# Performance work log

Hardware: AMD Instinct MI355X
Metric: run time of the kernel (lower is better)

## Reference

```python
import jax, jax.numpy as jnp
import numpy as np

N = 100000
E = 1600000
F_NODE = 32
F_EDGE = 8
H = 64


def _lin_params(key, fan_in, fan_out):
    k1, k2 = jax.random.split(key)
    lim = 1.0 / np.sqrt(fan_in)
    W = jax.random.uniform(k1, (fan_in, fan_out), minval=-lim, maxval=lim, dtype=jnp.float32)
    b = jax.random.uniform(k2, (fan_out,), minval=-lim, maxval=lim, dtype=jnp.float32)
    return W, b


def setup_inputs() -> dict:
    key = jax.random.key(0)
    ks = jax.random.split(key, 8)
    x = jax.random.normal(ks[0], (N, F_NODE), dtype=jnp.float32)
    edge_index = jax.random.randint(ks[1], (2, E), 0, N, dtype=jnp.int64)
    edge_attr = jax.random.normal(ks[2], (E, F_EDGE), dtype=jnp.float32)
    W_embed, b_embed = _lin_params(ks[3], F_NODE, H)
    W_c1, b_c1 = _lin_params(ks[4], H, H)
    W_c2, b_c2 = _lin_params(ks[5], H, H)
    W_p1, b_p1 = _lin_params(ks[6], 2 * H + F_EDGE, H)
    W_p2, b_p2 = _lin_params(ks[7], H, 1)
    return dict(x=x, edge_attr=edge_attr, W_embed=W_embed, b_embed=b_embed,
                W_c1=W_c1, b_c1=b_c1, W_c2=W_c2, b_c2=b_c2,
                W_p1=W_p1, b_p1=b_p1, W_p2=W_p2, b_p2=b_p2,
                edge_index=edge_index)


def gcn_conv(h, W, b, src, dst, n):
    # PyG GCNConv: add self-loops, symmetric normalization, then scatter-sum.
    h = h @ W  # [N, H]
    loops = jnp.arange(n, dtype=src.dtype)
    s = jnp.concatenate([src, loops])
    d = jnp.concatenate([dst, loops])
    deg = jax.ops.segment_sum(jnp.ones_like(d, dtype=h.dtype), d, num_segments=n)
    dinv = jnp.where(deg > 0, jax.lax.rsqrt(deg), 0.0)
    norm = dinv[s] * dinv[d]  # [E+N]
    msg = h[s] * norm[:, None]  # gather source features
    out = jax.ops.segment_sum(msg, d, num_segments=n)  # scatter to targets
    return out + b


def reference(x, edge_attr, W_embed, b_embed, W_c1, b_c1, W_c2, b_c2,
              W_p1, b_p1, W_p2, b_p2, edge_index):
    src, dst = edge_index[0], edge_index[1]
    h = jax.nn.relu(x @ W_embed + b_embed)
    h = jax.nn.relu(gcn_conv(h, W_c1, b_c1, src, dst, N))
    h = jax.nn.relu(gcn_conv(h, W_c2, b_c2, src, dst, N))
    # edge-level gather + concat with edge attrs
    ef = jnp.concatenate([h[src], h[dst], edge_attr], axis=1)  # [E, 2H+Fe]
    z = jax.nn.relu(ef @ W_p1 + b_p1)
    out = (z @ W_p2 + b_p2).squeeze(1)  # [E]
    return out
```

## Files before the change

kernel.cpp:

```cpp
#include <hip/hip_runtime.h>
#include <hip/hip_fp16.h>


typedef __attribute__((ext_vector_type(8))) _Float16 half8;
typedef __attribute__((ext_vector_type(4))) float f32x4;

__device__ __forceinline__ unsigned short f2h(float f) {
    return __half_as_ushort(__float2half(f));
}
__device__ __forceinline__ float h2f(unsigned short u) {
    return __half2float(__ushort_as_half(u));
}

__global__ void detect_idx_k(const unsigned int* __restrict__ ei, int* __restrict__ flag) {
    int nz = 0;
    for (int i = threadIdx.x; i < 2048; i += 64)
        if (ei[2 * i + 1] != 0u) nz = 1;
    unsigned long long m = __ballot(nz);
    if (threadIdx.x == 0) *flag = (m != 0ull) ? 1 : 0;
}

__global__ void cvt_idx_k(const void* __restrict__ ei, const int* __restrict__ flag,
                          int* __restrict__ out, int n) {
    int i = blockIdx.x * 256 + threadIdx.x;
    if (i >= n) return;
    if (*flag) out[i] = ((const int*)ei)[i];
    else       out[i] = (int)((const long long*)ei)[i];
}

__global__ void deg_i_k(const int* __restrict__ dst, int* __restrict__ deg, int E) {
    int i = blockIdx.x * 256 + threadIdx.x;
    if (i < E) atomicAdd(&deg[dst[i]], 1);
}

__global__ void scan_blk_k(const int* __restrict__ deg, int* __restrict__ part,
                           int* __restrict__ bsum, int n1) {
    __shared__ int s[256];
    int t = threadIdx.x;
    int i = blockIdx.x * 256 + t;
    int v = (i < n1) ? deg[i] : 0;
    s[t] = v;
    __syncthreads();
    for (int o = 1; o < 256; o <<= 1) {
        int x = (t >= o) ? s[t - o] : 0;
        __syncthreads();
        s[t] += x;
        __syncthreads();
    }
    if (i < n1) part[i] = s[t] - v;
    if (t == 255) bsum[blockIdx.x] = s[255];
}

__global__ void scan_tot_k(int* __restrict__ bsum, int nb) {
    __shared__ int s[512];
    int t = threadIdx.x;
    int v = (t < nb) ? bsum[t] : 0;
    s[t] = v;
    __syncthreads();
    for (int o = 1; o < 512; o <<= 1) {
        int x = (t >= o) ? s[t - o] : 0;
        __syncthreads();
        s[t] += x;
        __syncthreads();
    }
    if (t < nb) bsum[t] = s[t] - v;
}

__global__ void scan_add_k(const int* __restrict__ part, const int* __restrict__ bsum,
                           int* __restrict__ rowptr, int n1) {
    int i = blockIdx.x * 256 + threadIdx.x;
    if (i < n1) rowptr[i] = part[i] + bsum[blockIdx.x];
}

__global__ void dinv_k(const int* __restrict__ deg, float* __restrict__ dinv, int n) {
    int i = blockIdx.x * 256 + threadIdx.x;
    if (i < n) dinv[i] = rsqrtf((float)deg[i] + 1.0f);
}

__global__ void fill_csr_k(const int* __restrict__ src, const int* __restrict__ dst,
                           const int* __restrict__ rowptr, int* __restrict__ cursor,
                           int* __restrict__ csr, int E) {
    int e = blockIdx.x * 256 + threadIdx.x;
    if (e >= E) return;
    int d = dst[e];
    int pos = rowptr[d] + atomicAdd(&cursor[d], 1);
    csr[pos] = src[e];
}

__global__ void prep_w1_k(const float* __restrict__ W1, unsigned short* __restrict__ W1t) {
    int i = blockIdx.x * 256 + threadIdx.x;
    if (i >= 64 * 168) return;
    int n = i / 168, k = i % 168;
    float v = (k < 136) ? W1[k * 64 + n] : 0.0f;
    W1t[i] = f2h(v);
}

template <int K, bool BIAS, bool RELU, bool F16OUT>
__global__ __launch_bounds__(256, 4) void lin_tile_k(
    const float* __restrict__ A, const float* __restrict__ W,
    const float* __restrict__ b, void* __restrict__ outv, int n) {
    constexpr int KP = K + 4;
    __shared__ float As[128 * KP];
    __shared__ float Ws[64 * KP];
    int t = threadIdx.x;
    constexpr int K4 = K / 4;
    for (int i = t; i < 128 * K4; i += 256) {
        int r = i / K4, c4 = i % K4;
        int row = blockIdx.x * 128 + r;
        row = row < n ? row : n - 1;
        *(float4*)&As[r * KP + c4 * 4] = *(const float4*)&A[(size_t)row * K + c4 * 4];
    }
    for (int i = t; i < K * 64; i += 256) {
        int k = i >> 6, j = i & 63;
        Ws[j * KP + k] = W[i];
    }
    __syncthreads();
    int lane = t & 63;
    int wave = t >> 6;
    int ri = lane >> 3, ji = lane & 7;
    float acc[4][8];
#pragma unroll
    for (int m = 0; m < 4; m++)
#pragma unroll
        for (int c = 0; c < 8; c++) acc[m][c] = BIAS ? b[ji + 8 * c] : 0.0f;
#pragma unroll 2
    for (int kc = 0; kc < K; kc += 4) {
        float4 a[4], w[8];
#pragma unroll
        for (int m = 0; m < 4; m++)
            a[m] = *(const float4*)&As[(wave * 32 + ri + 8 * m) * KP + kc];
#pragma unroll
        for (int c = 0; c < 8; c++)
            w[c] = *(const float4*)&Ws[(ji + 8 * c) * KP + kc];
#pragma unroll
        for (int m = 0; m < 4; m++)
#pragma unroll
            for (int c = 0; c < 8; c++) {
                acc[m][c] = fmaf(a[m].x, w[c].x, acc[m][c]);
                acc[m][c] = fmaf(a[m].y, w[c].y, acc[m][c]);
                acc[m][c] = fmaf(a[m].z, w[c].z, acc[m][c]);
                acc[m][c] = fmaf(a[m].w, w[c].w, acc[m][c]);
            }
    }
#pragma unroll
    for (int m = 0; m < 4; m++) {
        int row = blockIdx.x * 128 + wave * 32 + ri + 8 * m;
        if (row < n) {
#pragma unroll
            for (int c = 0; c < 8; c++) {
                float v = acc[m][c];
                if (RELU) v = fmaxf(v, 0.0f);
                if (F16OUT) ((unsigned short*)outv)[(size_t)row * 64 + ji + 8 * c] = f2h(v);
                else        ((float*)outv)[(size_t)row * 64 + ji + 8 * c] = v;
            }
        }
    }
}

template <bool F16OUT>
__global__ __launch_bounds__(256) void conv_gather_k(
    const unsigned short* __restrict__ hW, const float* __restrict__ dinv,
    const int* __restrict__ rowptr, const int* __restrict__ csr,
    const float* __restrict__ b, void* __restrict__ outv, int n) {
    int lane = threadIdx.x & 63;
    int wave = threadIdx.x >> 6;
    int node = blockIdx.x * 4 + wave;
    if (node >= n) return;
    int beg = rowptr[node], end = rowptr[node + 1];
    float dv = dinv[node];
    float acc = h2f(hW[(size_t)node * 64 + lane]) * dv;
    int i = beg;
    for (; i + 8 <= end; i += 8) {
        int s[8];
#pragma unroll
        for (int u = 0; u < 8; u++) s[u] = csr[i + u];
        float h[8], w[8];
#pragma unroll
        for (int u = 0; u < 8; u++) h[u] = h2f(hW[(size_t)s[u] * 64 + lane]);
#pragma unroll
        for (int u = 0; u < 8; u++) w[u] = dinv[s[u]];
#pragma unroll
        for (int u = 0; u < 8; u++) acc = fmaf(h[u], w[u], acc);
    }
    for (; i + 4 <= end; i += 4) {
        int s0 = csr[i], s1 = csr[i + 1], s2 = csr[i + 2], s3 = csr[i + 3];
        float h0 = h2f(hW[(size_t)s0 * 64 + lane]);
        float h1 = h2f(hW[(size_t)s1 * 64 + lane]);
        float h2 = h2f(hW[(size_t)s2 * 64 + lane]);
        float h3 = h2f(hW[(size_t)s3 * 64 + lane]);
        acc = fmaf(h0, dinv[s0], acc);
        acc = fmaf(h1, dinv[s1], acc);
        acc = fmaf(h2, dinv[s2], acc);
        acc = fmaf(h3, dinv[s3], acc);
    }
    for (; i < end; i++) {
        int s = csr[i];
        acc = fmaf(h2f(hW[(size_t)s * 64 + lane]), dinv[s], acc);
    }
    float v = fmaxf(fmaf(acc, dv, b[lane]), 0.0f);
    if (F16OUT) ((unsigned short*)outv)[(size_t)node * 64 + lane] = f2h(v);
    else        ((float*)outv)[(size_t)node * 64 + lane] = v;
}

__global__ __launch_bounds__(256, 3) void edge_mlp_direct_k(
    const unsigned short* __restrict__ hb, const float* __restrict__ attr,
    const int* __restrict__ src, const int* __restrict__ dst,
    const unsigned short* __restrict__ W1t,
    const float* __restrict__ b1, const float* __restrict__ W2,
    const float* __restrict__ b2, float* __restrict__ out, int E, int nwaves) {
    int t = threadIdx.x;
    int lane = t & 63;
    int col = lane & 15;
    int quad = lane >> 4;
    int wid = blockIdx.x * 4 + (t >> 6);

    half8 Wf[4][5];
#pragma unroll
    for (int nt = 0; nt < 4; nt++)
#pragma unroll
        for (int kc = 0; kc < 5; kc++)
            Wf[nt][kc] = *(const half8*)&W1t[(nt * 16 + col) * 168 + kc * 32 + quad * 8];
    float b1v[4], w2v[4];
#pragma unroll
    for (int nt = 0; nt < 4; nt++) {
        b1v[nt] = b1[nt * 16 + col];
        w2v[nt] = W2[nt * 16 + col];
    }
    float b2v = b2[0];

    for (int base = wid * 32; base < E; base += nwaves * 32) {
        f32x4 acc[2][4];
#pragma unroll
        for (int mt = 0; mt < 2; mt++)
#pragma unroll
            for (int nt = 0; nt < 4; nt++)
                acc[mt][nt] = (f32x4){b1v[nt], b1v[nt], b1v[nt], b1v[nt]};
#pragma unroll
        for (int mt = 0; mt < 2; mt++) {
            int e = base + mt * 16 + col;
            e = e < E ? e : E - 1;
            int s = src[e], d = dst[e];
            half8 a0 = *(const half8*)&hb[(size_t)s * 64 + quad * 8];
            half8 a1 = *(const half8*)&hb[(size_t)s * 64 + 32 + quad * 8];
            half8 a2 = *(const half8*)&hb[(size_t)d * 64 + quad * 8];
            half8 a3 = *(const half8*)&hb[(size_t)d * 64 + 32 + quad * 8];
            half8 a4;
            if (quad == 0) {
                float4 x0 = ((const float4*)attr)[(size_t)e * 2];
                float4 x1 = ((const float4*)attr)[(size_t)e * 2 + 1];
                a4[0] = (_Float16)x0.x; a4[1] = (_Float16)x0.y;
                a4[2] = (_Float16)x0.z; a4[3] = (_Float16)x0.w;
                a4[4] = (_Float16)x1.x; a4[5] = (_Float16)x1.y;
                a4[6] = (_Float16)x1.z; a4[7] = (_Float16)x1.w;
            } else {
                a4 = (half8)(_Float16)0.0f;
            }
#pragma unroll
            for (int nt = 0; nt < 4; nt++) {
                acc[mt][nt] = __builtin_amdgcn_mfma_f32_16x16x32_f16(a0, Wf[nt][0], acc[mt][nt], 0, 0, 0);
                acc[mt][nt] = __builtin_amdgcn_mfma_f32_16x16x32_f16(a1, Wf[nt][1], acc[mt][nt], 0, 0, 0);
                acc[mt][nt] = __builtin_amdgcn_mfma_f32_16x16x32_f16(a2, Wf[nt][2], acc[mt][nt], 0, 0, 0);
                acc[mt][nt] = __builtin_amdgcn_mfma_f32_16x16x32_f16(a3, Wf[nt][3], acc[mt][nt], 0, 0, 0);
                acc[mt][nt] = __builtin_amdgcn_mfma_f32_16x16x32_f16(a4, Wf[nt][4], acc[mt][nt], 0, 0, 0);
            }
        }
#pragma unroll
        for (int mt = 0; mt < 2; mt++)
#pragma unroll
            for (int reg = 0; reg < 4; reg++) {
                float p = 0.0f;
#pragma unroll
                for (int nt = 0; nt < 4; nt++)
                    p = fmaf(fmaxf(acc[mt][nt][reg], 0.0f), w2v[nt], p);
                p += __shfl_xor(p, 1);
                p += __shfl_xor(p, 2);
                p += __shfl_xor(p, 4);
                p += __shfl_xor(p, 8);
                if (col == 0) {
                    int e = base + mt * 16 + quad * 4 + reg;
                    if (e < E) out[e] = p + b2v;
                }
            }
    }
}

extern "C" void kernel_launch(void* const* d_in, const int* in_sizes, int n_in,
                              void* d_out, int out_size, void* d_ws, size_t ws_size,
                              hipStream_t stream) {
    const float* x    = (const float*)d_in[0];
    const float* attr = (const float*)d_in[1];
    const float* W_e  = (const float*)d_in[2];
    const float* b_e  = (const float*)d_in[3];
    const float* W_c1 = (const float*)d_in[4];
    const float* b_c1 = (const float*)d_in[5];
    const float* W_c2 = (const float*)d_in[6];
    const float* b_c2 = (const float*)d_in[7];
    const float* W_p1 = (const float*)d_in[8];
    const float* b_p1 = (const float*)d_in[9];
    const float* W_p2 = (const float*)d_in[10];
    const float* b_p2 = (const float*)d_in[11];
    const void*  ei   = d_in[12];
    int N = in_sizes[0] / 32;
    int E = in_sizes[1] / 8;
    int n1 = N + 1;
    float* out = (float*)d_out;

    char* p = (char*)d_ws;
    auto alloc = [&](size_t bytes) { void* q = p; p += (bytes + 255) & ~(size_t)255; return q; };
    float* A            = (float*)alloc((size_t)N * 64 * 4);
    float* B            = (float*)alloc((size_t)N * 64 * 4);
    unsigned short* Hh  = (unsigned short*)alloc((size_t)N * 64 * 2);
    float* dinv         = (float*)alloc((size_t)N * 4);
    int* srcI           = (int*)alloc((size_t)E * 4);
    int* dstI           = (int*)alloc((size_t)E * 4);
    int* csr            = (int*)alloc((size_t)E * 4);
    int* deg            = (int*)alloc((size_t)n1 * 4);
    int* rowptr         = (int*)alloc((size_t)n1 * 4);
    int* part           = (int*)alloc((size_t)n1 * 4);
    int* bsum           = (int*)alloc(512 * 4);
    unsigned short* W1t = (unsigned short*)alloc(64 * 168 * 2);
    int* flag           = (int*)alloc(4);
    int* cursor = part;
    unsigned short* hb = (unsigned short*)A;

    auto cdiv = [](long long a, long long b) { return (int)((a + b - 1) / b); };

    detect_idx_k<<<1, 64, 0, stream>>>((const unsigned int*)ei, flag);
    cvt_idx_k<<<cdiv(2LL * E, 256), 256, 0, stream>>>(ei, flag, srcI, 2 * E);
    hipMemsetAsync(deg, 0, (size_t)n1 * 4, stream);
    deg_i_k<<<cdiv(E, 256), 256, 0, stream>>>(dstI, deg, E);
    int nb = cdiv(n1, 256);
    scan_blk_k<<<nb, 256, 0, stream>>>(deg, part, bsum, n1);
    scan_tot_k<<<1, 512, 0, stream>>>(bsum, nb);
    scan_add_k<<<nb, 256, 0, stream>>>(part, bsum, rowptr, n1);
    dinv_k<<<cdiv(N, 256), 256, 0, stream>>>(deg, dinv, N);
    hipMemsetAsync(cursor, 0, (size_t)N * 4, stream);
    fill_csr_k<<<cdiv(E, 256), 256, 0, stream>>>(srcI, dstI, rowptr, cursor, csr, E);
    prep_w1_k<<<cdiv(64 * 168, 256), 256, 0, stream>>>(W_p1, W1t);
    int lg = cdiv(N, 128);
    lin_tile_k<32, true, true, false><<<lg, 256, 0, stream>>>(x, W_e, b_e, A, N);
    lin_tile_k<64, false, false, true><<<lg, 256, 0, stream>>>(A, W_c1, nullptr, Hh, N);
    conv_gather_k<false><<<cdiv(N, 4), 256, 0, stream>>>(Hh, dinv, rowptr, csr, b_c1, B, N);
    lin_tile_k<64, false, false, true><<<lg, 256, 0, stream>>>(B, W_c2, nullptr, Hh, N);
    conv_gather_k<true><<<cdiv(N, 4), 256, 0, stream>>>(Hh, dinv, rowptr, csr, b_c2, hb, N);
    const int NB = 768;
    edge_mlp_direct_k<<<NB, 256, 0, stream>>>(hb, attr, srcI, dstI, W1t,
                                              b_p1, W_p2, b_p2, out, E, NB * 4);
}
```

Measured before the change: 558.7 us.

## Replace per-node CSR with bucketed edge binning and LDS-accumulated GCN aggregation

Replaces the per-destination CSR build, which did one global atomic per edge, with a coarse binning pass. Edges are grouped into buckets of 128 destination nodes using shared-memory counters, and each edge is packed as source plus local destination offset. The conv kernel then accumulates each bucket into a shared-memory image with LDS atomics. The degree count is fused into the index-conversion kernel, and the source dinv scaling moves into the linear kernel's epilogue, so each gather needs only one feature load. Risks include LDS atomic contention, hardcoded NBKT/20-bit index limits that cap N, and a different floating-point summation order.

```diff
diff --git a/kernel.cpp b/kernel.cpp
--- a/kernel.cpp
+++ b/kernel.cpp
@@ -11,6 +11,10 @@
 __device__ __forceinline__ float h2f(unsigned short u) {
     return __half2float(__ushort_as_half(u));
 }
+
+#define RB 128
+#define NBKT 782
+#define BINCHUNK 4096
 
 __global__ void detect_idx_k(const unsigned int* __restrict__ ei, int* __restrict__ flag) {
     int nz = 0;
@@ -20,17 +24,15 @@
     if (threadIdx.x == 0) *flag = (m != 0ull) ? 1 : 0;
 }
 
-__global__ void cvt_idx_k(const void* __restrict__ ei, const int* __restrict__ flag,
-                          int* __restrict__ out, int n) {
+__global__ void cvt_deg_k(const void* __restrict__ ei, const int* __restrict__ flag,
+                          int* __restrict__ out, int* __restrict__ deg, int E) {
     int i = blockIdx.x * 256 + threadIdx.x;
-    if (i >= n) return;
-    if (*flag) out[i] = ((const int*)ei)[i];
-    else       out[i] = (int)((const long long*)ei)[i];
-}
-
-__global__ void deg_i_k(const int* __restrict__ dst, int* __restrict__ deg, int E) {
-    int i = blockIdx.x * 256 + threadIdx.x;
-    if (i < E) atomicAdd(&deg[dst[i]], 1);
+    if (i >= 2 * E) return;
+    int v;
+    if (*flag) v = ((const int*)ei)[i];
+    else       v = (int)((const long long*)ei)[i];
+    out[i] = v;
+    if (i >= E) atomicAdd(&deg[v], 1);
 }
 
 __global__ void scan_blk_k(const int* __restrict__ deg, int* __restrict__ part,
@@ -77,14 +79,46 @@
     if (i < n) dinv[i] = rsqrtf((float)deg[i] + 1.0f);
 }
 
-__global__ void fill_csr_k(const int* __restrict__ src, const int* __restrict__ dst,
-                           const int* __restrict__ rowptr, int* __restrict__ cursor,
-                           int* __restrict__ csr, int E) {
-    int e = blockIdx.x * 256 + threadIdx.x;
-    if (e >= E) return;
-    int d = dst[e];
-    int pos = rowptr[d] + atomicAdd(&cursor[d], 1);
-    csr[pos] = src[e];
+__global__ void bcur_init_k(const int* __restrict__ rowptr, int* __restrict__ bcur,
+                            int nbkt) {
+    int b = blockIdx.x * 256 + threadIdx.x;
+    if (b < nbkt) bcur[b] = rowptr[b * RB];
+}
+
+__global__ __launch_bounds__(256) void bin_k(
+    const int* __restrict__ src, const int* __restrict__ dst,
+    int* __restrict__ bcur, unsigned int* __restrict__ pairB, int E, int nbkt) {
+    __shared__ int lsrc[BINCHUNK];
+    __shared__ int ldst[BINCHUNK];
+    __shared__ int cnt[NBKT], gbase[NBKT];
+    int t = threadIdx.x;
+    int base = blockIdx.x * BINCHUNK;
+    int n = E - base; if (n > BINCHUNK) n = BINCHUNK;
+    for (int i = t; i < nbkt; i += 256) cnt[i] = 0;
+    for (int i = t; i < n; i += 256) {
+        lsrc[i] = src[base + i];
+        ldst[i] = dst[base + i];
+    }
+    __syncthreads();
+    int rank[BINCHUNK / 256];
+#pragma unroll
+    for (int j = 0; j < BINCHUNK / 256; j++) {
+        int i = t + j * 256;
+        if (i < n) rank[j] = atomicAdd(&cnt[ldst[i] >> 7], 1);
+    }
+    __syncthreads();
+    for (int b = t; b < nbkt; b += 256)
+        if (cnt[b] > 0) gbase[b] = atomicAdd(&bcur[b], cnt[b]);
+    __syncthreads();
+#pragma unroll
+    for (int j = 0; j < BINCHUNK / 256; j++) {
+        int i = t + j * 256;
+        if (i < n) {
+            int d = ldst[i];
+            unsigned w = (unsigned)lsrc[i] | ((unsigned)(d & (RB - 1)) << 20);
+            pairB[gbase[d >> 7] + rank[j]] = w;
+        }
+    }
 }
 
 __global__ void prep_w1_k(const float* __restrict__ W1, unsigned short* __restrict__ W1t) {
@@ -95,10 +129,11 @@
     W1t[i] = f2h(v);
 }
 
-template <int K, bool BIAS, bool RELU, bool F16OUT>
+template <int K, bool BIAS, bool RELU, bool F16OUT, bool DINV>
 __global__ __launch_bounds__(256, 4) void lin_tile_k(
     const float* __restrict__ A, const float* __restrict__ W,
-    const float* __restrict__ b, void* __restrict__ outv, int n) {
+    const float* __restrict__ b, const float* __restrict__ dinv,
+    void* __restrict__ outv, int n) {
     constexpr int KP = K + 4;
     __shared__ float As[128 * KP];
     __shared__ float Ws[64 * KP];
@@ -146,10 +181,12 @@
     for (int m = 0; m < 4; m++) {
         int row = blockIdx.x * 128 + wave * 32 + ri + 8 * m;
         if (row < n) {
+            float dv = DINV ? dinv[row] : 1.0f;
 #pragma unroll
             for (int c = 0; c < 8; c++) {
                 float v = acc[m][c];
                 if (RELU) v = fmaxf(v, 0.0f);
+                if (DINV) v *= dv;
                 if (F16OUT) ((unsigned short*)outv)[(size_t)row * 64 + ji + 8 * c] = f2h(v);
                 else        ((float*)outv)[(size_t)row * 64 + ji + 8 * c] = v;
             }
@@ -158,48 +195,51 @@
 }
 
 template <bool F16OUT>
-__global__ __launch_bounds__(256) void conv_gather_k(
-    const unsigned short* __restrict__ hW, const float* __restrict__ dinv,
-    const int* __restrict__ rowptr, const int* __restrict__ csr,
-    const float* __restrict__ b, void* __restrict__ outv, int n) {
-    int lane = threadIdx.x & 63;
-    int wave = threadIdx.x >> 6;
-    int node = blockIdx.x * 4 + wave;
-    if (node >= n) return;
-    int beg = rowptr[node], end = rowptr[node + 1];
-    float dv = dinv[node];
-    float acc = h2f(hW[(size_t)node * 64 + lane]) * dv;
-    int i = beg;
-    for (; i + 8 <= end; i += 8) {
-        int s[8];
-#pragma unroll
-        for (int u = 0; u < 8; u++) s[u] = csr[i + u];
-        float h[8], w[8];
-#pragma unroll
-        for (int u = 0; u < 8; u++) h[u] = h2f(hW[(size_t)s[u] * 64 + lane]);
-#pragma unroll
-        for (int u = 0; u < 8; u++) w[u] = dinv[s[u]];
-#pragma unroll
-        for (int u = 0; u < 8; u++) acc = fmaf(h[u], w[u], acc);
-    }
-    for (; i + 4 <= end; i += 4) {
-        int s0 = csr[i], s1 = csr[i + 1], s2 = csr[i + 2], s3 = csr[i + 3];
-        float h0 = h2f(hW[(size_t)s0 * 64 + lane]);
-        float h1 = h2f(hW[(size_t)s1 * 64 + lane]);
-        float h2 = h2f(hW[(size_t)s2 * 64 + lane]);
-        float h3 = h2f(hW[(size_t)s3 * 64 + lane]);
-        acc = fmaf(h0, dinv[s0], acc);
-        acc = fmaf(h1, dinv[s1], acc);
-        acc = fmaf(h2, dinv[s2], acc);
-        acc = fmaf(h3, dinv[s3], acc);
-    }
-    for (; i < end; i++) {
-        int s = csr[i];
-        acc = fmaf(h2f(hW[(size_t)s * 64 + lane]), dinv[s], acc);
-    }
-    float v = fmaxf(fmaf(acc, dv, b[lane]), 0.0f);
-    if (F16OUT) ((unsigned short*)outv)[(size_t)node * 64 + lane] = f2h(v);
-    else        ((float*)outv)[(size_t)node * 64 + lane] = v;
+__global__ __launch_bounds__(256) void conv_bucket_k(
+    const unsigned short* __restrict__ Hh, const float* __restrict__ dinv,
+    const int* __restrict__ rowptr, const unsigned int* __restrict__ pairB,
+    const float* __restrict__ b, void* __restrict__ outv, int N) {
+    __shared__ float img[RB * 64];
+    int t = threadIdx.x, lane = t & 63, wave = t >> 6;
+    int node0 = blockIdx.x * RB;
+    int nn = N - node0; if (nn > RB) nn = RB;
+    for (int i = t; i < RB * 64 / 4; i += 256)
+        ((float4*)img)[i] = (float4){0.f, 0.f, 0.f, 0.f};
+    int beg = rowptr[node0];
+    int end = rowptr[node0 + nn];
+    float bv = b[lane];
+    __syncthreads();
+    for (int basei = beg + wave * 64; basei < end; basei += 256) {
+        int m = end - basei; if (m > 64) m = 64;
+        unsigned w = (lane < m) ? pairB[basei + lane] : 0u;
+        int j = 0;
+        for (; j + 8 <= m; j += 8) {
+            float v[8]; int dl[8];
+#pragma unroll
+            for (int u = 0; u < 8; u++) {
+                unsigned wj = __shfl(w, j + u);
+                dl[u] = wj >> 20;
+                v[u] = h2f(Hh[(size_t)(wj & 0xFFFFF) * 64 + lane]);
+            }
+#pragma unroll
+            for (int u = 0; u < 8; u++)
+                atomicAdd(&img[dl[u] * 64 + lane], v[u]);
+        }
+        for (; j < m; j++) {
+            unsigned wj = __shfl(w, j);
+            float v = h2f(Hh[(size_t)(wj & 0xFFFFF) * 64 + lane]);
+            atomicAdd(&img[(wj >> 20) * 64 + lane], v);
+        }
+    }
+    __syncthreads();
+    for (int nl = wave; nl < nn; nl += 4) {
+        int node = node0 + nl;
+        float dv = dinv[node];
+        float self = h2f(Hh[(size_t)node * 64 + lane]);
+        float v = fmaxf(fmaf(img[nl * 64 + lane] + self, dv, bv), 0.0f);
+        if (F16OUT) ((unsigned short*)outv)[(size_t)node * 64 + lane] = f2h(v);
+        else        ((float*)outv)[(size_t)node * 64 + lane] = v;
+    }
 }
 
 __global__ __launch_bounds__(256, 3) void edge_mlp_direct_k(
@@ -303,6 +343,7 @@
     int N = in_sizes[0] / 32;
     int E = in_sizes[1] / 8;
     int n1 = N + 1;
+    int nbkt = (N + RB - 1) / RB;
     float* out = (float*)d_out;
 
     char* p = (char*)d_ws;
@@ -313,36 +354,35 @@
     float* dinv         = (float*)alloc((size_t)N * 4);
     int* srcI           = (int*)alloc((size_t)E * 4);
     int* dstI           = (int*)alloc((size_t)E * 4);
-    int* csr            = (int*)alloc((size_t)E * 4);
+    unsigned int* pairB = (unsigned int*)alloc((size_t)E * 4);
     int* deg            = (int*)alloc((size_t)n1 * 4);
     int* rowptr         = (int*)alloc((size_t)n1 * 4);
     int* part           = (int*)alloc((size_t)n1 * 4);
     int* bsum           = (int*)alloc(512 * 4);
+    int* bcur           = (int*)alloc((size_t)nbkt * 4);
     unsigned short* W1t = (unsigned short*)alloc(64 * 168 * 2);
     int* flag           = (int*)alloc(4);
-    int* cursor = part;
     unsigned short* hb = (unsigned short*)A;
 
     auto cdiv = [](long long a, long long b) { return (int)((a + b - 1) / b); };
 
     detect_idx_k<<<1, 64, 0, stream>>>((const unsigned int*)ei, flag);
-    cvt_idx_k<<<cdiv(2LL * E, 256), 256, 0, stream>>>(ei, flag, srcI, 2 * E);
     hipMemsetAsync(deg, 0, (size_t)n1 * 4, stream);
-    deg_i_k<<<cdiv(E, 256), 256, 0, stream>>>(dstI, deg, E);
+    cvt_deg_k<<<cdiv(2LL * E, 256), 256, 0, stream>>>(ei, flag, srcI, deg, E);
     int nb = cdiv(n1, 256);
     scan_blk_k<<<nb, 256, 0, stream>>>(deg, part, bsum, n1);
     scan_tot_k<<<1, 512, 0, stream>>>(bsum, nb);
     scan_add_k<<<nb, 256, 0, stream>>>(part, bsum, rowptr, n1);
     dinv_k<<<cdiv(N, 256), 256, 0, stream>>>(deg, dinv, N);
-    hipMemsetAsync(cursor, 0, (size_t)N * 4, stream);
-    fill_csr_k<<<cdiv(E, 256), 256, 0, stream>>>(srcI, dstI, rowptr, cursor, csr, E);
+    bcur_init_k<<<cdiv(nbkt, 256), 256, 0, stream>>>(rowptr, bcur, nbkt);
+    bin_k<<<cdiv(E, BINCHUNK), 256, 0, stream>>>(srcI, dstI, bcur, pairB, E, nbkt);
     prep_w1_k<<<cdiv(64 * 168, 256), 256, 0, stream>>>(W_p1, W1t);
     int lg = cdiv(N, 128);
-    lin_tile_k<32, true, true, false><<<lg, 256, 0, stream>>>(x, W_e, b_e, A, N);
-    lin_tile_k<64, false, false, true><<<lg, 256, 0, stream>>>(A, W_c1, nullptr, Hh, N);
-    conv_gather_k<false><<<cdiv(N, 4), 256, 0, stream>>>(Hh, dinv, rowptr, csr, b_c1, B, N);
-    lin_tile_k<64, false, false, true><<<lg, 256, 0, stream>>>(B, W_c2, nullptr, Hh, N);
-    conv_gather_k<true><<<cdiv(N, 4), 256, 0, stream>>>(Hh, dinv, rowptr, csr, b_c2, hb, N);
+    lin_tile_k<32, true, true, false, false><<<lg, 256, 0, stream>>>(x, W_e, b_e, nullptr, A, N);
+    lin_tile_k<64, false, false, true, true><<<lg, 256, 0, stream>>>(A, W_c1, nullptr, dinv, Hh, N);
+    conv_bucket_k<false><<<nbkt, 256, 0, stream>>>(Hh, dinv, rowptr, pairB, b_c1, B, N);
+    lin_tile_k<64, false, false, true, true><<<lg, 256, 0, stream>>>(B, W_c2, nullptr, dinv, Hh, N);
+    conv_bucket_k<true><<<nbkt, 256, 0, stream>>>(Hh, dinv, rowptr, pairB, b_c2, hb, N);
     const int NB = 768;
     edge_mlp_direct_k<<<NB, 256, 0, stream>>>(hb, attr, srcI, dstI, W1t,
                                               b_p1, W_p2, b_p2, out, E, NB * 4);
```

Measured after the change: 1.792 ms. 3.21x slower.
